# Kernel tuning notes

Hardware: AMD Instinct MI355X
Metric: run time of the kernel (lower is better)

## Reference

```python
import jax, jax.numpy as jnp
import numpy as np

N_NODES = 50000
N_EDGES = 800000
N_GRAPHS = 64
D_IN, D_HID, D_OUT = 128, 128, 64


def setup_inputs() -> dict:
    key = jax.random.key(0)
    ks = jax.random.split(key, 9)
    s = 0.05
    return {
        "x": jax.random.normal(ks[0], (N_NODES, D_IN), jnp.float32),
        "edge_index": jax.random.randint(ks[1], (2, N_EDGES), 0, N_NODES, dtype=jnp.int64),
        "batch": jnp.sort(jax.random.randint(ks[2], (N_NODES,), 0, N_GRAPHS, dtype=jnp.int64)),
        "W1": jax.random.normal(ks[3], (D_IN, D_HID), jnp.float32) * s,
        "b1": jnp.zeros((D_HID,), jnp.float32),
        "W2": jax.random.normal(ks[4], (D_HID, D_HID), jnp.float32) * s,
        "b2": jnp.zeros((D_HID,), jnp.float32),
        "W3": jax.random.normal(ks[5], (D_HID, D_OUT), jnp.float32) * s,
        "b3": jnp.zeros((D_OUT,), jnp.float32),
    }


def _gcn_conv(x, W, b, src, dst, dinv, n_nodes):
    # PyG GCNConv: h = X W; out = sum_{j->i} norm_ij h_j + self-loop term + b
    h = x @ W
    norm_e = dinv[src] * dinv[dst]                      # [E]
    agg = jax.ops.segment_sum(norm_e[:, None] * h[src], dst, num_segments=n_nodes)
    agg = agg + (dinv * dinv)[:, None] * h              # self-loop (norm = dinv_i^2)
    return agg + b


def reference(x, edge_index, batch, W1, b1, W2, b2, W3, b3):
    n_nodes = x.shape[0]
    src, dst = edge_index[0], edge_index[1]
    # symmetric normalization with self-loops: deg_i = in_degree_i + 1
    deg = jax.ops.segment_sum(jnp.ones_like(dst, dtype=x.dtype), dst, num_segments=n_nodes) + 1.0
    dinv = jax.lax.rsqrt(deg)

    h = jax.nn.relu(_gcn_conv(x, W1, b1, src, dst, dinv, n_nodes))
    h = jax.nn.relu(_gcn_conv(h, W2, b2, src, dst, dinv, n_nodes))
    h = _gcn_conv(h, W3, b3, src, dst, dinv, n_nodes)

    # global_mean_pool over graph id
    sums = jax.ops.segment_sum(h, batch, num_segments=N_GRAPHS)
    counts = jax.ops.segment_sum(jnp.ones((n_nodes,), h.dtype), batch, num_segments=N_GRAPHS)
    return sums / jnp.maximum(counts, 1.0)[:, None]
```

## Files before the change

kernel.cpp:

```cpp
#include <hip/hip_runtime.h>

#define NN 50000
#define NE 800000
#define NG 64
#define NCHUNK 64
#define CHUNK 12500
#define HALF 25000

typedef short short8 __attribute__((ext_vector_type(8)));
typedef float f32x4 __attribute__((ext_vector_type(4)));

__device__ __forceinline__ unsigned short f2bf(float f) {
    unsigned int u = __float_as_uint(f);
    u = (u + 0x7FFFu + ((u >> 16) & 1u)) >> 16;
    return (unsigned short)u;
}
__device__ __forceinline__ float bf2f(unsigned short h) {
    return __uint_as_float((unsigned int)h << 16);
}
__device__ __forceinline__ void fma8(float* acc, float w, const uint4 v) {
    const unsigned int u0 = v.x, u1 = v.y, u2 = v.z, u3 = v.w;
    acc[0] = fmaf(w, __uint_as_float(u0 << 16), acc[0]);
    acc[1] = fmaf(w, __uint_as_float(u0 & 0xFFFF0000u), acc[1]);
    acc[2] = fmaf(w, __uint_as_float(u1 << 16), acc[2]);
    acc[3] = fmaf(w, __uint_as_float(u1 & 0xFFFF0000u), acc[3]);
    acc[4] = fmaf(w, __uint_as_float(u2 << 16), acc[4]);
    acc[5] = fmaf(w, __uint_as_float(u2 & 0xFFFF0000u), acc[5]);
    acc[6] = fmaf(w, __uint_as_float(u3 << 16), acc[6]);
    acc[7] = fmaf(w, __uint_as_float(u3 & 0xFFFF0000u), acc[7]);
}

__global__ __launch_bounds__(1024) void k_hist(const int* __restrict__ ei,
                                               unsigned short* __restrict__ rank,
                                               unsigned short* __restrict__ percnt) {
    __shared__ unsigned int cnt[HALF / 2];
    const int b = blockIdx.x;
    const int dbase = blockIdx.y * HALF;
    const int tid = threadIdx.x;
    for (int i = tid; i < HALF / 2; i += 1024) cnt[i] = 0;
    __syncthreads();
    const int e0 = b * CHUNK;
    for (int i = tid; i < CHUNK; i += 1024) {
        const int d = ei[NE + e0 + i];
        const int local = d - dbase;
        if ((unsigned)local < (unsigned)HALF) {
            const unsigned int old = atomicAdd(&cnt[local >> 1], 1u << ((local & 1) * 16));
            rank[e0 + i] = (unsigned short)((old >> ((local & 1) * 16)) & 0xFFFFu);
        }
    }
    __syncthreads();
    unsigned int* dst = (unsigned int*)&percnt[(size_t)b * NN + dbase];
    for (int i = tid; i < HALF / 2; i += 1024) dst[i] = cnt[i];
}

__global__ __launch_bounds__(256) void k_colscan(unsigned short* __restrict__ percnt,
                                                 int* __restrict__ degcnt, float* __restrict__ dinv) {
    const int d = blockIdx.x * 256 + threadIdx.x;
    if (d >= NN) return;
    int acc = 0;
#pragma unroll 8
    for (int b = 0; b < NCHUNK; ++b) {
        const int c = percnt[(size_t)b * NN + d];
        percnt[(size_t)b * NN + d] = (unsigned short)acc;
        acc += c;
    }
    degcnt[d] = acc;
    dinv[d] = (float)(1.0 / sqrt((double)acc + 1.0));
}

__global__ __launch_bounds__(1024) void k_scan1(const int* __restrict__ cnt, int* __restrict__ row_ptr,
                                                int* __restrict__ blk_sums) {
    __shared__ int s[1024];
    const int tid = threadIdx.x;
    const int i = blockIdx.x * 1024 + tid;
    int v = (i < NN) ? cnt[i] : 0;
    s[tid] = v;
    __syncthreads();
    for (int off = 1; off < 1024; off <<= 1) {
        int t = (tid >= off) ? s[tid - off] : 0;
        __syncthreads();
        s[tid] += t;
        __syncthreads();
    }
    if (i < NN) row_ptr[i] = s[tid] - v;
    if (tid == 1023) blk_sums[blockIdx.x] = s[1023];
}

__global__ __launch_bounds__(64) void k_scan2(int* __restrict__ blk_sums, int nb) {
    int l = threadIdx.x;
    int v = (l < nb) ? blk_sums[l] : 0;
    int incl = v;
    for (int off = 1; off < 64; off <<= 1) {
        int t = __shfl_up(incl, off, 64);
        if (l >= off) incl += t;
    }
    if (l < nb) blk_sums[l] = incl - v;
}

__global__ __launch_bounds__(1024) void k_scan3(int* __restrict__ row_ptr, const int* __restrict__ blk_sums) {
    int i = blockIdx.x * 1024 + threadIdx.x;
    if (i < NN) row_ptr[i] += blk_sums[blockIdx.x];
    if (i == 0) row_ptr[NN] = NE;
}

__global__ __launch_bounds__(256) void k_fill3(const int* __restrict__ ei, const int* __restrict__ row_ptr,
                                               const unsigned short* __restrict__ rank,
                                               const unsigned short* __restrict__ offs,
                                               int* __restrict__ csr_src) {
    const int e = blockIdx.x * 256 + threadIdx.x;
    if (e >= NE) return;
    const int s = ei[e];
    const int d = ei[NE + e];
    const int b = e / CHUNK;
    const int pos = row_ptr[d] + (int)offs[(size_t)b * NN + d] + (int)rank[e];
    csr_src[pos] = s;
}

__global__ __launch_bounds__(256) void k_cvtx(const float* __restrict__ x, unsigned short* __restrict__ xb) {
    const size_t t = (size_t)blockIdx.x * 256 + threadIdx.x;
    const size_t base = t * 8;
    if (base >= (size_t)NN * 128) return;
    const float4 a = *(const float4*)&x[base];
    const float4 b = *(const float4*)&x[base + 4];
    uint4 o;
    o.x = (unsigned int)f2bf(a.x) | ((unsigned int)f2bf(a.y) << 16);
    o.y = (unsigned int)f2bf(a.z) | ((unsigned int)f2bf(a.w) << 16);
    o.z = (unsigned int)f2bf(b.x) | ((unsigned int)f2bf(b.y) << 16);
    o.w = (unsigned int)f2bf(b.z) | ((unsigned int)f2bf(b.w) << 16);
    *(uint4*)&xb[base] = o;
}

__global__ __launch_bounds__(1024) void k_cvtw(const float* __restrict__ W1, const float* __restrict__ W2,
                                               const float* __restrict__ W3,
                                               unsigned short* __restrict__ wt1, unsigned short* __restrict__ wt2,
                                               unsigned short* __restrict__ wt3) {
    const int m = blockIdx.x;
    const float* W = (m == 0) ? W1 : (m == 1) ? W2 : W3;
    unsigned short* O = (m == 0) ? wt1 : (m == 1) ? wt2 : wt3;
    const int DO = (m == 2) ? 64 : 128;
    const int total = DO * 128;
    for (int o = threadIdx.x; o < total; o += 1024) {
        const int n = o >> 7;
        const int k = o & 127;
        O[o] = f2bf(W[(size_t)k * DO + n]);
    }
}

template <int DO>
__global__ __launch_bounds__(256) void k_gemm_mfma(const unsigned short* __restrict__ A,
                                                   const unsigned short* __restrict__ WtG,
                                                   unsigned short* __restrict__ C, int M) {
    constexpr int NT = DO / 16;
    constexpr int LDK = 136;
    __shared__ __align__(16) unsigned short As[64 * LDK];
    __shared__ __align__(16) unsigned short Ws[DO * LDK];
    const int tid = threadIdx.x;
    const int row0 = blockIdx.x * 64;

    for (int task = tid; task < DO * 16; task += 256) {
        const int n = task >> 4;
        const int ko = (task & 15) * 8;
        *(uint4*)&Ws[n * LDK + ko] = *(const uint4*)&WtG[(size_t)n * 128 + ko];
    }
    {
        const int r = tid >> 2;
        const int c0 = (tid & 3) * 32;
        const int grow = row0 + r;
#pragma unroll
        for (int q = 0; q < 4; ++q) {
            uint4 v = make_uint4(0, 0, 0, 0);
            if (grow < M) v = *(const uint4*)&A[(size_t)grow * 128 + c0 + q * 8];
            *(uint4*)&As[r * LDK + c0 + q * 8] = v;
        }
    }
    __syncthreads();

    const int l = tid & 63;
    const int w = tid >> 6;
    const int lr = l & 15;
    const int lg = l >> 4;
    f32x4 acc[NT];
#pragma unroll
    for (int nt = 0; nt < NT; ++nt) acc[nt] = (f32x4){0.f, 0.f, 0.f, 0.f};

#pragma unroll
    for (int kk = 0; kk < 128; kk += 32) {
        const short8 af = *(const short8*)&As[(w * 16 + lr) * LDK + kk + lg * 8];
#pragma unroll
        for (int nt = 0; nt < NT; ++nt) {
            const short8 bfv = *(const short8*)&Ws[(nt * 16 + lr) * LDK + kk + lg * 8];
            acc[nt] = __builtin_amdgcn_mfma_f32_16x16x32_bf16(af, bfv, acc[nt], 0, 0, 0);
        }
    }

#pragma unroll
    for (int nt = 0; nt < NT; ++nt) {
#pragma unroll
        for (int r = 0; r < 4; ++r) {
            const int grow = row0 + w * 16 + lg * 4 + r;
            if (grow < M) C[(size_t)grow * DO + nt * 16 + lr] = f2bf(acc[nt][r]);
        }
    }
}

template <int D, bool RELU>
__global__ __launch_bounds__(256) void k_agg(const unsigned short* __restrict__ T, const float* __restrict__ bias,
                                             const float* __restrict__ dinv, const int* __restrict__ row_ptr,
                                             const int* __restrict__ csr_src,
                                             unsigned short* __restrict__ out) {
    constexpr int G = D / 8;
    constexpr int NPB = 256 / G;
    const int tid = threadIdx.x;
    const int lane = tid % G;
    const int grp = tid / G;
    const int n = blockIdx.x * NPB + grp;
    if (n >= NN) return;
    const int f0 = lane * 8;

    const float di_n = dinv[n];
    float acc[8] = {0.f, 0.f, 0.f, 0.f, 0.f, 0.f, 0.f, 0.f};
    const int beg = row_ptr[n];
    const int end = row_ptr[n + 1];
    int e = beg;
    for (; e + 8 <= end; e += 8) {
        int s[8];
        float wv[8];
#pragma unroll
        for (int j = 0; j < 8; ++j) s[j] = csr_src[e + j];
#pragma unroll
        for (int j = 0; j < 8; ++j) wv[j] = dinv[s[j]] * di_n;
        uint4 v[8];
#pragma unroll
        for (int j = 0; j < 8; ++j) v[j] = *(const uint4*)&T[(size_t)s[j] * D + f0];
#pragma unroll
        for (int j = 0; j < 8; ++j) fma8(acc, wv[j], v[j]);
    }
    for (; e + 4 <= end; e += 4) {
        const int s0 = csr_src[e + 0], s1 = csr_src[e + 1], s2 = csr_src[e + 2], s3 = csr_src[e + 3];
        const float w0 = dinv[s0] * di_n, w1 = dinv[s1] * di_n, w2 = dinv[s2] * di_n, w3 = dinv[s3] * di_n;
        const uint4 v0 = *(const uint4*)&T[(size_t)s0 * D + f0];
        const uint4 v1 = *(const uint4*)&T[(size_t)s1 * D + f0];
        const uint4 v2 = *(const uint4*)&T[(size_t)s2 * D + f0];
        const uint4 v3 = *(const uint4*)&T[(size_t)s3 * D + f0];
        fma8(acc, w0, v0);
        fma8(acc, w1, v1);
        fma8(acc, w2, v2);
        fma8(acc, w3, v3);
    }
    for (; e < end; ++e) {
        const int s = csr_src[e];
        const float w = dinv[s] * di_n;
        const uint4 v = *(const uint4*)&T[(size_t)s * D + f0];
        fma8(acc, w, v);
    }
    {
        const uint4 v = *(const uint4*)&T[(size_t)n * D + f0];
        fma8(acc, di_n * di_n, v);
    }
    const float4 b0 = *(const float4*)&bias[f0];
    const float4 b1 = *(const float4*)&bias[f0 + 4];
    acc[0] += b0.x; acc[1] += b0.y; acc[2] += b0.z; acc[3] += b0.w;
    acc[4] += b1.x; acc[5] += b1.y; acc[6] += b1.z; acc[7] += b1.w;
    if (RELU) {
#pragma unroll
        for (int j = 0; j < 8; ++j) acc[j] = fmaxf(acc[j], 0.f);
    }
    uint4 o;
    o.x = (unsigned int)f2bf(acc[0]) | ((unsigned int)f2bf(acc[1]) << 16);
    o.y = (unsigned int)f2bf(acc[2]) | ((unsigned int)f2bf(acc[3]) << 16);
    o.z = (unsigned int)f2bf(acc[4]) | ((unsigned int)f2bf(acc[5]) << 16);
    o.w = (unsigned int)f2bf(acc[6]) | ((unsigned int)f2bf(acc[7]) << 16);
    *(uint4*)&out[(size_t)n * D + f0] = o;
}

__global__ __launch_bounds__(256) void k_pool(const unsigned short* __restrict__ h, const int* __restrict__ batch,
                                              double* __restrict__ sums, int* __restrict__ cnts) {
    const int NB = 256;
    const int n0 = blockIdx.x * NB;
    const int d = threadIdx.x & 63;
    const int sub = threadIdx.x >> 6;
    double acc = 0.0;
    int cnt = 0;
    int cur = -1;
    for (int i = sub; i < NB; i += 4) {
        int n = n0 + i;
        if (n >= NN) break;
        int g = batch[n];
        if (g != cur) {
            if (cur >= 0) {
                atomicAdd(&sums[cur * 64 + d], acc);
                if (d == 0) atomicAdd(&cnts[cur], cnt);
            }
            cur = g;
            acc = 0.0;
            cnt = 0;
        }
        acc += (double)bf2f(h[(size_t)n * 64 + d]);
        cnt++;
    }
    if (cur >= 0) {
        atomicAdd(&sums[cur * 64 + d], acc);
        if (d == 0) atomicAdd(&cnts[cur], cnt);
    }
}

__global__ __launch_bounds__(256) void k_final(const double* __restrict__ sums, const int* __restrict__ cnts,
                                               float* __restrict__ out) {
    int i = blockIdx.x * 256 + threadIdx.x;
    if (i >= NG * 64) return;
    int g = i >> 6;
    double c = (double)max(cnts[g], 1);
    out[i] = (float)(sums[i] / c);
}

extern "C" void kernel_launch(void* const* d_in, const int* in_sizes, int n_in,
                              void* d_out, int out_size, void* d_ws, size_t ws_size,
                              hipStream_t stream) {
    (void)in_sizes; (void)n_in; (void)out_size; (void)ws_size;
    const float* x     = (const float*)d_in[0];
    const int*   ei    = (const int*)d_in[1];
    const int*   batch = (const int*)d_in[2];
    const float* W1    = (const float*)d_in[3];
    const float* b1    = (const float*)d_in[4];
    const float* W2    = (const float*)d_in[5];
    const float* b2    = (const float*)d_in[6];
    const float* W3    = (const float*)d_in[7];
    const float* b3    = (const float*)d_in[8];
    float* out = (float*)d_out;

    char* w = (char*)d_ws;
    char*  zbase = w;
    double* psums  = (double*)w;        w += (size_t)NG * 64 * 8;
    int*    pcnts  = (int*)w;           w += 256;
    size_t zbytes = (size_t)(w - zbase);
    int*    degcnt = (int*)w;           w += (size_t)NN * 4;
    float*  dinv   = (float*)w;         w += (size_t)NN * 4;
    int*    row_ptr = (int*)w;          w += (size_t)(NN + 4) * 4;
    int*    blk_sums = (int*)w;         w += 64 * 4;
    unsigned short* wt1 = (unsigned short*)w;  w += 128 * 128 * 2;
    unsigned short* wt2 = (unsigned short*)w;  w += 128 * 128 * 2;
    unsigned short* wt3 = (unsigned short*)w;  w += 64 * 128 * 2;
    unsigned short* rank   = (unsigned short*)w;  w += (size_t)NE * 2;
    unsigned short* percnt = (unsigned short*)w;  w += (size_t)NCHUNK * NN * 2;
    int*    csr_src = (int*)w;          w += (size_t)NE * 4;
    unsigned short* xb   = (unsigned short*)w;  w += (size_t)NN * 128 * 2;
    unsigned short* bufT = (unsigned short*)w;  w += (size_t)NN * 128 * 2;
    unsigned short* bufA = (unsigned short*)w;  w += (size_t)NN * 128 * 2;

    hipMemsetAsync(zbase, 0, zbytes, stream);

    k_cvtx<<<3125, 256, 0, stream>>>(x, xb);
    k_cvtw<<<3, 1024, 0, stream>>>(W1, W2, W3, wt1, wt2, wt3);
    k_hist<<<dim3(NCHUNK, 2), 1024, 0, stream>>>(ei, rank, percnt);
    k_colscan<<<(NN + 255) / 256, 256, 0, stream>>>(percnt, degcnt, dinv);
    const int nb_scan = (NN + 1023) / 1024;
    k_scan1<<<nb_scan, 1024, 0, stream>>>(degcnt, row_ptr, blk_sums);
    k_scan2<<<1, 64, 0, stream>>>(blk_sums, nb_scan);
    k_scan3<<<nb_scan, 1024, 0, stream>>>(row_ptr, blk_sums);
    k_fill3<<<(NE + 255) / 256, 256, 0, stream>>>(ei, row_ptr, rank, percnt, csr_src);

    const int gemm_grid = (NN + 63) / 64;
    const int agg_grid128 = (NN + 15) / 16;
    const int agg_grid64  = (NN + 31) / 32;
    k_gemm_mfma<128><<<gemm_grid, 256, 0, stream>>>(xb, wt1, bufT, NN);
    k_agg<128, true><<<agg_grid128, 256, 0, stream>>>(bufT, b1, dinv, row_ptr, csr_src, bufA);
    k_gemm_mfma<128><<<gemm_grid, 256, 0, stream>>>(bufA, wt2, bufT, NN);
    k_agg<128, true><<<agg_grid128, 256, 0, stream>>>(bufT, b2, dinv, row_ptr, csr_src, bufA);
    k_gemm_mfma<64><<<gemm_grid, 256, 0, stream>>>(bufA, wt3, bufT, NN);
    k_agg<64, false><<<agg_grid64, 256, 0, stream>>>(bufT, b3, dinv, row_ptr, csr_src, bufA);
    k_pool<<<(NN + 255) / 256, 256, 0, stream>>>(bufA, batch, psums, pcnts);
    k_final<<<(NG * 64 + 255) / 256, 256, 0, stream>>>(psums, pcnts, out);
}
```

Baseline: 239.2 us.

## Fuse preprocessing kernels and use last-block patterns to cut launches

Merges the memset, x conversion, weight conversion and histogram into one multi-role kernel, k_prep. The three-kernel row_ptr scan moves into k_colscan's last block through an atomic done counter, and the final mean division moves into k_pool's last block the same way. This removes several kernel launches and their gaps. In exchange, the row_ptr scan now runs serially in a single 256-thread block over 50k entries, and correctness depends on threadfence and atomic-counter ordering.

```diff
diff --git a/kernel.cpp b/kernel.cpp
--- a/kernel.cpp
+++ b/kernel.cpp
@@ -30,77 +30,111 @@
     acc[7] = fmaf(w, __uint_as_float(u3 & 0xFFFF0000u), acc[7]);
 }
 
-__global__ __launch_bounds__(1024) void k_hist(const int* __restrict__ ei,
+__global__ __launch_bounds__(1024) void k_prep(const float* __restrict__ x, const float* __restrict__ W1,
+                                               const float* __restrict__ W2, const float* __restrict__ W3,
+                                               const int* __restrict__ ei,
+                                               unsigned short* __restrict__ xb,
+                                               unsigned short* __restrict__ wt1, unsigned short* __restrict__ wt2,
+                                               unsigned short* __restrict__ wt3,
                                                unsigned short* __restrict__ rank,
-                                               unsigned short* __restrict__ percnt) {
+                                               unsigned short* __restrict__ percnt,
+                                               unsigned int* __restrict__ zwords, int nzw) {
     __shared__ unsigned int cnt[HALF / 2];
     const int b = blockIdx.x;
-    const int dbase = blockIdx.y * HALF;
-    const int tid = threadIdx.x;
-    for (int i = tid; i < HALF / 2; i += 1024) cnt[i] = 0;
+    const int tid = threadIdx.x;
+    if (b < 128) {
+        const int chunk = b & 63;
+        const int dbase = (b >> 6) * HALF;
+        for (int i = tid; i < HALF / 2; i += 1024) cnt[i] = 0;
+        __syncthreads();
+        const int e0 = chunk * CHUNK;
+        for (int i = tid; i < CHUNK; i += 1024) {
+            const int d = ei[NE + e0 + i];
+            const int local = d - dbase;
+            if ((unsigned)local < (unsigned)HALF) {
+                const unsigned int old = atomicAdd(&cnt[local >> 1], 1u << ((local & 1) * 16));
+                rank[e0 + i] = (unsigned short)((old >> ((local & 1) * 16)) & 0xFFFFu);
+            }
+        }
+        __syncthreads();
+        unsigned int* dst = (unsigned int*)&percnt[(size_t)chunk * NN + dbase];
+        for (int i = tid; i < HALF / 2; i += 1024) dst[i] = cnt[i];
+    } else if (b < 910) {
+        const size_t base = ((size_t)(b - 128) * 1024 + tid) * 8;
+        if (base < (size_t)NN * 128) {
+            const float4 a = *(const float4*)&x[base];
+            const float4 c = *(const float4*)&x[base + 4];
+            uint4 o;
+            o.x = (unsigned int)f2bf(a.x) | ((unsigned int)f2bf(a.y) << 16);
+            o.y = (unsigned int)f2bf(a.z) | ((unsigned int)f2bf(a.w) << 16);
+            o.z = (unsigned int)f2bf(c.x) | ((unsigned int)f2bf(c.y) << 16);
+            o.w = (unsigned int)f2bf(c.z) | ((unsigned int)f2bf(c.w) << 16);
+            *(uint4*)&xb[base] = o;
+        }
+    } else if (b == 910) {
+        for (int o = tid; o < 128 * 128; o += 1024) {
+            const int n = o >> 7;
+            const int k = o & 127;
+            wt1[o] = f2bf(W1[(size_t)k * 128 + n]);
+            wt2[o] = f2bf(W2[(size_t)k * 128 + n]);
+        }
+        for (int o = tid; o < 64 * 128; o += 1024) {
+            const int n = o >> 7;
+            const int k = o & 127;
+            wt3[o] = f2bf(W3[(size_t)k * 64 + n]);
+        }
+    } else {
+        for (int i = tid; i < nzw; i += 1024) zwords[i] = 0;
+    }
+}
+
+__global__ __launch_bounds__(256) void k_colscan(unsigned short* __restrict__ percnt,
+                                                 int* __restrict__ degcnt, float* __restrict__ dinv,
+                                                 int* __restrict__ row_ptr, int* __restrict__ done) {
+    const int tid = threadIdx.x;
+    const int d = blockIdx.x * 256 + tid;
+    if (d < NN) {
+        int acc = 0;
+#pragma unroll 8
+        for (int b = 0; b < NCHUNK; ++b) {
+            const int c = percnt[(size_t)b * NN + d];
+            percnt[(size_t)b * NN + d] = (unsigned short)acc;
+            acc += c;
+        }
+        degcnt[d] = acc;
+        dinv[d] = (float)(1.0 / sqrt((double)acc + 1.0));
+    }
+    __threadfence();
+    __shared__ int lastFlag;
+    if (tid == 0) lastFlag = (atomicAdd(done, 1) == (int)gridDim.x - 1) ? 1 : 0;
     __syncthreads();
-    const int e0 = b * CHUNK;
-    for (int i = tid; i < CHUNK; i += 1024) {
-        const int d = ei[NE + e0 + i];
-        const int local = d - dbase;
-        if ((unsigned)local < (unsigned)HALF) {
-            const unsigned int old = atomicAdd(&cnt[local >> 1], 1u << ((local & 1) * 16));
-            rank[e0 + i] = (unsigned short)((old >> ((local & 1) * 16)) & 0xFFFFu);
-        }
-    }
+    if (!lastFlag) return;
+    __threadfence();
+    constexpr int PER = (NN + 255) / 256;
+    const int base = tid * PER;
+    int sum = 0;
+    for (int i = 0; i < PER; ++i) {
+        const int idx = base + i;
+        if (idx < NN) sum += degcnt[idx];
+    }
+    __shared__ int ps[256];
+    ps[tid] = sum;
     __syncthreads();
-    unsigned int* dst = (unsigned int*)&percnt[(size_t)b * NN + dbase];
-    for (int i = tid; i < HALF / 2; i += 1024) dst[i] = cnt[i];
-}
-
-__global__ __launch_bounds__(256) void k_colscan(unsigned short* __restrict__ percnt,
-                                                 int* __restrict__ degcnt, float* __restrict__ dinv) {
-    const int d = blockIdx.x * 256 + threadIdx.x;
-    if (d >= NN) return;
-    int acc = 0;
-#pragma unroll 8
-    for (int b = 0; b < NCHUNK; ++b) {
-        const int c = percnt[(size_t)b * NN + d];
-        percnt[(size_t)b * NN + d] = (unsigned short)acc;
-        acc += c;
-    }
-    degcnt[d] = acc;
-    dinv[d] = (float)(1.0 / sqrt((double)acc + 1.0));
-}
-
-__global__ __launch_bounds__(1024) void k_scan1(const int* __restrict__ cnt, int* __restrict__ row_ptr,
-                                                int* __restrict__ blk_sums) {
-    __shared__ int s[1024];
-    const int tid = threadIdx.x;
-    const int i = blockIdx.x * 1024 + tid;
-    int v = (i < NN) ? cnt[i] : 0;
-    s[tid] = v;
-    __syncthreads();
-    for (int off = 1; off < 1024; off <<= 1) {
-        int t = (tid >= off) ? s[tid - off] : 0;
+    for (int off = 1; off < 256; off <<= 1) {
+        const int t = (tid >= off) ? ps[tid - off] : 0;
         __syncthreads();
-        s[tid] += t;
+        ps[tid] += t;
         __syncthreads();
     }
-    if (i < NN) row_ptr[i] = s[tid] - v;
-    if (tid == 1023) blk_sums[blockIdx.x] = s[1023];
-}
-
-__global__ __launch_bounds__(64) void k_scan2(int* __restrict__ blk_sums, int nb) {
-    int l = threadIdx.x;
-    int v = (l < nb) ? blk_sums[l] : 0;
-    int incl = v;
-    for (int off = 1; off < 64; off <<= 1) {
-        int t = __shfl_up(incl, off, 64);
-        if (l >= off) incl += t;
-    }
-    if (l < nb) blk_sums[l] = incl - v;
-}
-
-__global__ __launch_bounds__(1024) void k_scan3(int* __restrict__ row_ptr, const int* __restrict__ blk_sums) {
-    int i = blockIdx.x * 1024 + threadIdx.x;
-    if (i < NN) row_ptr[i] += blk_sums[blockIdx.x];
-    if (i == 0) row_ptr[NN] = NE;
+    int run = ps[tid] - sum;
+    for (int i = 0; i < PER; ++i) {
+        const int idx = base + i;
+        if (idx < NN) {
+            row_ptr[idx] = run;
+            run += degcnt[idx];
+        }
+    }
+    if (tid == 0) row_ptr[NN] = NE;
 }
 
 __global__ __launch_bounds__(256) void k_fill3(const int* __restrict__ ei, const int* __restrict__ row_ptr,
@@ -116,36 +150,6 @@
     csr_src[pos] = s;
 }
 
-__global__ __launch_bounds__(256) void k_cvtx(const float* __restrict__ x, unsigned short* __restrict__ xb) {
-    const size_t t = (size_t)blockIdx.x * 256 + threadIdx.x;
-    const size_t base = t * 8;
-    if (base >= (size_t)NN * 128) return;
-    const float4 a = *(const float4*)&x[base];
-    const float4 b = *(const float4*)&x[base + 4];
-    uint4 o;
-    o.x = (unsigned int)f2bf(a.x) | ((unsigned int)f2bf(a.y) << 16);
-    o.y = (unsigned int)f2bf(a.z) | ((unsigned int)f2bf(a.w) << 16);
-    o.z = (unsigned int)f2bf(b.x) | ((unsigned int)f2bf(b.y) << 16);
-    o.w = (unsigned int)f2bf(b.z) | ((unsigned int)f2bf(b.w) << 16);
-    *(uint4*)&xb[base] = o;
-}
-
-__global__ __launch_bounds__(1024) void k_cvtw(const float* __restrict__ W1, const float* __restrict__ W2,
-                                               const float* __restrict__ W3,
-                                               unsigned short* __restrict__ wt1, unsigned short* __restrict__ wt2,
-                                               unsigned short* __restrict__ wt3) {
-    const int m = blockIdx.x;
-    const float* W = (m == 0) ? W1 : (m == 1) ? W2 : W3;
-    unsigned short* O = (m == 0) ? wt1 : (m == 1) ? wt2 : wt3;
-    const int DO = (m == 2) ? 64 : 128;
-    const int total = DO * 128;
-    for (int o = threadIdx.x; o < total; o += 1024) {
-        const int n = o >> 7;
-        const int k = o & 127;
-        O[o] = f2bf(W[(size_t)k * DO + n]);
-    }
-}
-
 template <int DO>
 __global__ __launch_bounds__(256) void k_gemm_mfma(const unsigned short* __restrict__ A,
                                                    const unsigned short* __restrict__ WtG,
@@ -274,11 +278,13 @@
 }
 
 __global__ __launch_bounds__(256) void k_pool(const unsigned short* __restrict__ h, const int* __restrict__ batch,
-                                              double* __restrict__ sums, int* __restrict__ cnts) {
+                                              double* __restrict__ sums, int* __restrict__ cnts,
+                                              int* __restrict__ done, float* __restrict__ out) {
     const int NB = 256;
     const int n0 = blockIdx.x * NB;
-    const int d = threadIdx.x & 63;
-    const int sub = threadIdx.x >> 6;
+    const int tid = threadIdx.x;
+    const int d = tid & 63;
+    const int sub = tid >> 6;
     double acc = 0.0;
     int cnt = 0;
     int cur = -1;
@@ -302,15 +308,16 @@
         atomicAdd(&sums[cur * 64 + d], acc);
         if (d == 0) atomicAdd(&cnts[cur], cnt);
     }
-}
-
-__global__ __launch_bounds__(256) void k_final(const double* __restrict__ sums, const int* __restrict__ cnts,
-                                               float* __restrict__ out) {
-    int i = blockIdx.x * 256 + threadIdx.x;
-    if (i >= NG * 64) return;
-    int g = i >> 6;
-    double c = (double)max(cnts[g], 1);
-    out[i] = (float)(sums[i] / c);
+    __threadfence();
+    __shared__ int lastFlag;
+    if (tid == 0) lastFlag = (atomicAdd(done, 1) == (int)gridDim.x - 1) ? 1 : 0;
+    __syncthreads();
+    if (!lastFlag) return;
+    __threadfence();
+    for (int i = tid; i < NG * 64; i += 256) {
+        const double c = (double)max(cnts[i >> 6], 1);
+        out[i] = (float)(sums[i] / c);
+    }
 }
 
 extern "C" void kernel_launch(void* const* d_in, const int* in_sizes, int n_in,
@@ -332,11 +339,11 @@
     char*  zbase = w;
     double* psums  = (double*)w;        w += (size_t)NG * 64 * 8;
     int*    pcnts  = (int*)w;           w += 256;
-    size_t zbytes = (size_t)(w - zbase);
+    int*    dflags = (int*)w;           w += 256;
+    const int nzw = (int)((w - zbase) / 4);
     int*    degcnt = (int*)w;           w += (size_t)NN * 4;
     float*  dinv   = (float*)w;         w += (size_t)NN * 4;
     int*    row_ptr = (int*)w;          w += (size_t)(NN + 4) * 4;
-    int*    blk_sums = (int*)w;         w += 64 * 4;
     unsigned short* wt1 = (unsigned short*)w;  w += 128 * 128 * 2;
     unsigned short* wt2 = (unsigned short*)w;  w += 128 * 128 * 2;
     unsigned short* wt3 = (unsigned short*)w;  w += 64 * 128 * 2;
@@ -347,16 +354,9 @@
     unsigned short* bufT = (unsigned short*)w;  w += (size_t)NN * 128 * 2;
     unsigned short* bufA = (unsigned short*)w;  w += (size_t)NN * 128 * 2;
 
-    hipMemsetAsync(zbase, 0, zbytes, stream);
-
-    k_cvtx<<<3125, 256, 0, stream>>>(x, xb);
-    k_cvtw<<<3, 1024, 0, stream>>>(W1, W2, W3, wt1, wt2, wt3);
-    k_hist<<<dim3(NCHUNK, 2), 1024, 0, stream>>>(ei, rank, percnt);
-    k_colscan<<<(NN + 255) / 256, 256, 0, stream>>>(percnt, degcnt, dinv);
-    const int nb_scan = (NN + 1023) / 1024;
-    k_scan1<<<nb_scan, 1024, 0, stream>>>(degcnt, row_ptr, blk_sums);
-    k_scan2<<<1, 64, 0, stream>>>(blk_sums, nb_scan);
-    k_scan3<<<nb_scan, 1024, 0, stream>>>(row_ptr, blk_sums);
+    k_prep<<<912, 1024, 0, stream>>>(x, W1, W2, W3, ei, xb, wt1, wt2, wt3, rank, percnt,
+                                     (unsigned int*)zbase, nzw);
+    k_colscan<<<(NN + 255) / 256, 256, 0, stream>>>(percnt, degcnt, dinv, row_ptr, &dflags[0]);
     k_fill3<<<(NE + 255) / 256, 256, 0, stream>>>(ei, row_ptr, rank, percnt, csr_src);
 
     const int gemm_grid = (NN + 63) / 64;
@@ -368,6 +368,5 @@
     k_agg<128, true><<<agg_grid128, 256, 0, stream>>>(bufT, b2, dinv, row_ptr, csr_src, bufA);
     k_gemm_mfma<64><<<gemm_grid, 256, 0, stream>>>(bufA, wt3, bufT, NN);
     k_agg<64, false><<<agg_grid64, 256, 0, stream>>>(bufT, b3, dinv, row_ptr, csr_src, bufA);
-    k_pool<<<(NN + 255) / 256, 256, 0, stream>>>(bufA, batch, psums, pcnts);
-    k_final<<<(NG * 64 + 255) / 256, 256, 0, stream>>>(psums, pcnts, out);
-}
+    k_pool<<<(NN + 255) / 256, 256, 0, stream>>>(bufA, batch, psums, pcnts, &dflags[1], out);
+}
```

Result: slower. 359.3 us (+50.2%).
